# Optimization experiments

Measured on AMD Instinct MI355X. Metric: run time of the kernel, lower is better.

The kernel has to match this reference:

```python
import jax, jax.numpy as jnp
from jax import lax
import numpy as np


def _greedy_match(s):
    """Sequential greedy assignment on a single [N, N] score matrix.
    Mirrors Binary.forward for the n1=n2=None (square) case:
    repeat N times: pick global argmax, zero its row and column in the
    working copy, set perm[row, col] = 1.
    """
    N = s.shape[0]

    def step(carry, _):
        s_tmp, perm = carry
        idx = jnp.argmax(s_tmp)          # flat argmax over N*N
        r = idx // N
        c = idx % N
        s_tmp = s_tmp.at[r, :].set(0.0).at[:, c].set(0.0)
        perm = perm.at[r, c].set(1.0)
        return (s_tmp, perm), None

    (_, perm), _ = lax.scan(step, (s, jnp.zeros_like(s)), None, length=N)
    return perm


def setup_inputs() -> dict:
    key = jax.random.key(0)
    B, N = 256, 512
    s = jax.random.uniform(key, (B, N, N), dtype=jnp.float32)
    return {"s": s}


def reference(s):
    # vmap over batch; each batch element runs an independent sequential
    # greedy matching (the data-dependent part is the length-N scan).
    return jax.vmap(_greedy_match)(s)
```

## Files before the change

### kernel.cpp

```cpp
#include <hip/hip_runtime.h>

#define NN 512
#define BATCH 256
#define T 8
#define ATH 40

typedef unsigned long long u64;
typedef unsigned u32;
typedef unsigned char u8;
typedef unsigned short u16;

#define DEADK 512ull
#define LIVEMIN (1ull << 32)
#define UNKNOWN 0xFFFFu

__device__ __forceinline__ u64 fm(u64 a, u64 b) {
    return (u64)__double_as_longlong(fmax(__longlong_as_double((long long)a),
                                          __longlong_as_double((long long)b)));
}
__device__ __forceinline__ u64 fmn(u64 a, u64 b) {
    return (u64)__double_as_longlong(fmin(__longlong_as_double((long long)a),
                                          __longlong_as_double((long long)b)));
}

#define DPP_FMAX64(k, ctrl) do {                                              \
    int _lo = (int)(u32)(k); int _hi = (int)((k) >> 32);                      \
    int _olo = __builtin_amdgcn_update_dpp(_lo, _lo, ctrl, 0xf, 0xf, false);  \
    int _ohi = __builtin_amdgcn_update_dpp(_hi, _hi, ctrl, 0xf, 0xf, false);  \
    u64 _o = ((u64)(u32)_ohi << 32) | (u32)_olo;                              \
    (k) = fm((k), _o);                                                        \
} while (0)

#define WAVE_FMAX64(k) do {                                                   \
    DPP_FMAX64(k, 0x111); DPP_FMAX64(k, 0x112); DPP_FMAX64(k, 0x114);         \
    DPP_FMAX64(k, 0x118); DPP_FMAX64(k, 0x142); DPP_FMAX64(k, 0x143);         \
} while (0)

__device__ __forceinline__ u64 readlane64(u64 k, int l) {
    u32 lo = (u32)__builtin_amdgcn_readlane((int)(u32)k, l);
    u32 hi = (u32)__builtin_amdgcn_readlane((int)(k >> 32), l);
    return ((u64)hi << 32) | lo;
}

__device__ __forceinline__ u64 amsel(int w, u64 a0, u64 a1, u64 a2, u64 a3,
                                     u64 a4, u64 a5, u64 a6, u64 a7) {
    u64 x01 = (w & 1) ? a1 : a0;
    u64 x23 = (w & 1) ? a3 : a2;
    u64 x45 = (w & 1) ? a5 : a4;
    u64 x67 = (w & 1) ? a7 : a6;
    u64 y0 = (w & 2) ? x23 : x01;
    u64 y1 = (w & 2) ? x67 : x45;
    return (w & 4) ? y1 : y0;
}

#define INS8(X, A0, A1, A2, A3, A4, A5, A6, A7) do {                          \
    u64 _x = (X), _n;                                                         \
    _n = fm(A0, _x); _x = fmn(A0, _x); A0 = _n;                               \
    _n = fm(A1, _x); _x = fmn(A1, _x); A1 = _n;                               \
    _n = fm(A2, _x); _x = fmn(A2, _x); A2 = _n;                               \
    _n = fm(A3, _x); _x = fmn(A3, _x); A3 = _n;                               \
    _n = fm(A4, _x); _x = fmn(A4, _x); A4 = _n;                               \
    _n = fm(A5, _x); _x = fmn(A5, _x); A5 = _n;                               \
    _n = fm(A6, _x); _x = fmn(A6, _x); A6 = _n;                               \
    A7 = fm(A7, _x);                                                          \
} while (0)

#define ALIVE_C(cc) ((amsel((int)(cc) >> 6, am0,am1,am2,am3,am4,am5,am6,am7)  \
                      >> ((cc) & 63)) & 1ull)
#define ALIVE_R(rr) ((amsel((int)(rr) >> 6, ar0,ar1,ar2,ar3,ar4,ar5,ar6,ar7)  \
                      >> ((rr) & 63)) & 1ull)
#define SETK(RS, VAL) do {                                                    \
        const int rsl_ = (RS) & 63, rsj_ = (RS) >> 6;                         \
        const bool mn_ = (lane == rsl_);                                      \
        k0 = (mn_ && rsj_ == 0) ? (VAL) : k0;                                 \
        k1 = (mn_ && rsj_ == 1) ? (VAL) : k1;                                 \
        k2 = (mn_ && rsj_ == 2) ? (VAL) : k2;                                 \
        k3 = (mn_ && rsj_ == 3) ? (VAL) : k3;                                 \
        k4 = (mn_ && rsj_ == 4) ? (VAL) : k4;                                 \
        k5 = (mn_ && rsj_ == 5) ? (VAL) : k5;                                 \
        k6 = (mn_ && rsj_ == 6) ? (VAL) : k6;                                 \
        k7 = (mn_ && rsj_ == 7) ? (VAL) : k7;                                 \
    } while (0)

#define COLDROW(RR, NKVAR) do {                                               \
        const float* rp_ = sb + (size_t)(RR) * NN;                            \
        const float4 fa_ = *(const float4*)(rp_ + 4 * lane);                  \
        const float4 fv_ = *(const float4*)(rp_ + 256 + 4 * lane);            \
        const int sh_ = (4 * lane) & 63; const int wq_ = lane >> 4;           \
        u64 xlo_ = (wq_ == 0) ? am0 : (wq_ == 1) ? am1 : (wq_ == 2) ? am2 : am3; \
        u64 xhi_ = (wq_ == 0) ? am4 : (wq_ == 1) ? am5 : (wq_ == 2) ? am6 : am7; \
        const u32 al8_ = ((u32)(xlo_ >> sh_) & 0xFu)                          \
                       | (((u32)(xhi_ >> sh_) & 0xFu) << 4);                  \
        u64 e0_ = (al8_ & 1u)   ? ((((u64)__float_as_uint(fa_.x) + 1) << 9) | (u32)(511 - (4*lane+0))) : 0; \
        u64 e1_ = (al8_ & 2u)   ? ((((u64)__float_as_uint(fa_.y) + 1) << 9) | (u32)(511 - (4*lane+1))) : 0; \
        u64 e2_ = (al8_ & 4u)   ? ((((u64)__float_as_uint(fa_.z) + 1) << 9) | (u32)(511 - (4*lane+2))) : 0; \
        u64 e3_ = (al8_ & 8u)   ? ((((u64)__float_as_uint(fa_.w) + 1) << 9) | (u32)(511 - (4*lane+3))) : 0; \
        u64 e4_ = (al8_ & 16u)  ? ((((u64)__float_as_uint(fv_.x) + 1) << 9) | (u32)(511 - (256+4*lane+0))) : 0; \
        u64 e5_ = (al8_ & 32u)  ? ((((u64)__float_as_uint(fv_.y) + 1) << 9) | (u32)(511 - (256+4*lane+1))) : 0; \
        u64 e6_ = (al8_ & 64u)  ? ((((u64)__float_as_uint(fv_.z) + 1) << 9) | (u32)(511 - (256+4*lane+2))) : 0; \
        u64 e7_ = (al8_ & 128u) ? ((((u64)__float_as_uint(fv_.w) + 1) << 9) | (u32)(511 - (256+4*lane+3))) : 0; \
        u64 n0_ = fm(e0_, e1_), n1_ = fm(e2_, e3_);                           \
        u64 n2_ = fm(e4_, e5_), n3_ = fm(e6_, e7_);                           \
        n0_ = fm(n0_, n1_); n2_ = fm(n2_, n3_);                               \
        u64 bw_ = fm(n0_, n2_);                                               \
        WAVE_FMAX64(bw_);                                                     \
        bw_ = readlane64(bw_, 63);                                            \
        const int wc_ = 511 - (int)(bw_ & 511);                               \
        NKVAR = ((bw_ >> 9) << 32)                                            \
              | ((u64)(u32)(512 - (RR)) << 16) | (u32)wc_;                    \
        if (lane == 0)                                                        \
            rl[RR][7] = (((bw_ >> 9) - 1ull) << 32) | (u32)wc_;               \
    } while (0)

__global__ __launch_bounds__(256) void build_row(const float* __restrict__ s,
                                                 float* __restrict__ out) {
    const int b = blockIdx.x >> 3;
    const int rbase = (blockIdx.x & 7) * 64;
    const int t = threadIdx.x;
    const int ct = t & 63, q = t >> 6;

    __shared__ float tile[64][65];
    __shared__ u64 mrg[64][4][8];

    const float* sb = s + (size_t)b * NN * NN;

    u64 t0 = 0, t1 = 0, t2 = 0, t3 = 0, t4 = 0, t5 = 0, t6 = 0, t7 = 0;

    for (int ch = 0; ch < 8; ++ch) {
        const int cbase = ch * 64;
        #pragma unroll
        for (int i = 0; i < 16; ++i) {
            const int rr = q + 4 * i;
            tile[rr][ct] = sb[(size_t)(rbase + rr) * NN + cbase + ct];
        }
        __syncthreads();
        #pragma unroll
        for (int i = 0; i < 16; ++i) {
            const int cc = cbase + 16 * q + i;
            const float v = tile[ct][16 * q + i];
            const u64 x = (((u64)__float_as_uint(v) + 1) << 9) | (u32)(511 - cc);
            INS8(x, t0, t1, t2, t3, t4, t5, t6, t7);
        }
        __syncthreads();
    }

    mrg[ct][q][0] = t0;  mrg[ct][q][1] = t1;  mrg[ct][q][2] = t2;
    mrg[ct][q][3] = t3;  mrg[ct][q][4] = t4;  mrg[ct][q][5] = t5;
    mrg[ct][q][6] = t6;  mrg[ct][q][7] = t7;
    __syncthreads();

    if (t < 64) {
        u64 m0 = 0, m1 = 0, m2 = 0, m3 = 0, m4 = 0, m5 = 0, m6 = 0, m7 = 0;
        #pragma unroll
        for (int qq = 0; qq < 4; ++qq)
            #pragma unroll
            for (int ii = 0; ii < 8; ++ii) {
                const u64 x = mrg[t][qq][ii];
                INS8(x, m0, m1, m2, m3, m4, m5, m6, m7);
            }
        u64* dst = (u64*)(out + (size_t)b * NN * NN) + (size_t)(rbase + t) * T;
        dst[0] = (((m0 >> 9) - 1ull) << 32) | (u32)(511 - (int)(m0 & 511));
        dst[1] = (((m1 >> 9) - 1ull) << 32) | (u32)(511 - (int)(m1 & 511));
        dst[2] = (((m2 >> 9) - 1ull) << 32) | (u32)(511 - (int)(m2 & 511));
        dst[3] = (((m3 >> 9) - 1ull) << 32) | (u32)(511 - (int)(m3 & 511));
        dst[4] = (((m4 >> 9) - 1ull) << 32) | (u32)(511 - (int)(m4 & 511));
        dst[5] = (((m5 >> 9) - 1ull) << 32) | (u32)(511 - (int)(m5 & 511));
        dst[6] = (((m6 >> 9) - 1ull) << 32) | (u32)(511 - (int)(m6 & 511));
        dst[7] = (((m7 >> 9) - 1ull) << 32) | (u32)(511 - (int)(m7 & 511));
    }
}

__global__ __launch_bounds__(256) void build_col(const float* __restrict__ s,
                                                 float* __restrict__ out) {
    const int b = blockIdx.x >> 3;
    const int cbase = (blockIdx.x & 7) * 64;
    const int t = threadIdx.x;
    const int ct = t & 63, q = t >> 6;

    __shared__ float tile[64][65];
    __shared__ u64 mrg[64][4][8];

    const float* sb = s + (size_t)b * NN * NN;

    u64 t0 = 0, t1 = 0, t2 = 0, t3 = 0, t4 = 0, t5 = 0, t6 = 0, t7 = 0;

    for (int ch = 0; ch < 8; ++ch) {
        const int rbase = ch * 64;
        #pragma unroll
        for (int i = 0; i < 16; ++i) {
            const int rr = q + 4 * i;
            tile[rr][ct] = sb[(size_t)(rbase + rr) * NN + cbase + ct];
        }
        __syncthreads();
        #pragma unroll
        for (int i = 0; i < 16; ++i) {
            const int rr = rbase + q * 16 + i;
            const float v = tile[q * 16 + i][ct];
            const u64 x = (((u64)__float_as_uint(v) + 1) << 9) | (u32)(511 - rr);
            INS8(x, t0, t1, t2, t3, t4, t5, t6, t7);
        }
        __syncthreads();
    }

    mrg[ct][q][0] = t0;  mrg[ct][q][1] = t1;  mrg[ct][q][2] = t2;
    mrg[ct][q][3] = t3;  mrg[ct][q][4] = t4;  mrg[ct][q][5] = t5;
    mrg[ct][q][6] = t6;  mrg[ct][q][7] = t7;
    __syncthreads();

    if (t < 64) {
        u64 m0 = 0, m1 = 0, m2 = 0, m3 = 0, m4 = 0, m5 = 0, m6 = 0, m7 = 0;
        #pragma unroll
        for (int qq = 0; qq < 4; ++qq)
            #pragma unroll
            for (int ii = 0; ii < 8; ++ii) {
                const u64 x = mrg[t][qq][ii];
                INS8(x, m0, m1, m2, m3, m4, m5, m6, m7);
            }
        u64* dst = (u64*)(out + (size_t)b * NN * NN) + (size_t)NN * T
                 + (size_t)(cbase + t) * T;
        dst[0] = m0; dst[1] = m1; dst[2] = m2; dst[3] = m3;
        dst[4] = m4; dst[5] = m5; dst[6] = m6; dst[7] = m7;
    }
}

__global__ __launch_bounds__(256) void greedy_A(const float* __restrict__ s,
                                                float* __restrict__ out,
                                                u32* __restrict__ ws_mat) {
    __shared__ __align__(16) u64 rl[NN][9];
    __shared__ __align__(16) u64 cl[NN][9];
    __shared__ __align__(16) u64 keysL[NN];
    __shared__ u32 colh[NN];
    __shared__ u8 aliveR[NN];
    __shared__ u8 aliveC[NN];
    __shared__ u16 match16[NN];
    __shared__ int cntW[4];

    const int tid = threadIdx.x;
    const int w = tid >> 6, lane = tid & 63;
    const int b = blockIdx.x;
    const float* sb = s + (size_t)b * NN * NN;
    float* ob = out + (size_t)b * NN * NN;
    u64* st = (u64*)ob + 8192;

    {
        const ulonglong2* src = (const ulonglong2*)ob;
        #pragma unroll
        for (int i = 0; i < 8; ++i) {
            const int i2 = tid + 256 * i;
            const ulonglong2 vR = src[i2];
            const ulonglong2 vC = src[2048 + i2];
            const int idx = i2 * 2;
            rl[idx >> 3][idx & 7] = vR.x;  rl[idx >> 3][(idx & 7) + 1] = vR.y;
            cl[idx >> 3][idx & 7] = vC.x;  cl[idx >> 3][(idx & 7) + 1] = vC.y;
        }
    }
    if (tid < 128) {
        ((u32*)aliveR)[tid] = 0x01010101u;
        ((u32*)aliveC)[tid] = 0x01010101u;
    }
    match16[tid] = 0; match16[tid + 256] = 0;
    __syncthreads();
    #pragma unroll
    for (int i = 0; i < 2; ++i) {
        const int r = tid + 256 * i;
        const u64 e = rl[r][0];
        keysL[r] = (((e >> 32) + 1ull) << 32)
                 | ((u64)(u32)(512 - r) << 16) | (e & 511ull);
        colh[r] = 511u - ((u32)cl[r][0] & 511u);
    }
    __syncthreads();

    u64 am0 = ~0ull, am1 = ~0ull, am2 = ~0ull, am3 = ~0ull,
        am4 = ~0ull, am5 = ~0ull, am6 = ~0ull, am7 = ~0ull;
    u64 ar0 = ~0ull, ar1 = ~0ull, ar2 = ~0ull, ar3 = ~0ull,
        ar4 = ~0ull, ar5 = ~0ull, ar6 = ~0ull, ar7 = ~0ull;

    int alive = NN;

    #pragma unroll 1
    for (int round = 0; round < 64; ++round) {
        int part = 0;
        #pragma unroll
        for (int j = 0; j < 2; ++j) {
            const int row = 128 * w + 64 * j + lane;
            const u64 kj = keysL[row];
            const u32 cc = (u32)kj & 511u;
            const bool hit = (kj >= LIVEMIN) && (colh[cc] == (u32)row);
            part += (int)__builtin_popcountll(__ballot(hit));
            if (hit) {
                match16[row] = (u16)cc;
                aliveC[cc] = 0;
                aliveR[row] = 0;
                keysL[row] = DEADK;
            }
        }
        if (lane == 0) cntW[w] = part;
        __syncthreads();
        const int cnt = cntW[0] + cntW[1] + cntW[2] + cntW[3];
        if (cnt == 0) break;
        alive -= cnt;

        am0 = __ballot(aliveC[lane] != 0);        am1 = __ballot(aliveC[64 + lane] != 0);
        am2 = __ballot(aliveC[128 + lane] != 0);  am3 = __ballot(aliveC[192 + lane] != 0);
        am4 = __ballot(aliveC[256 + lane] != 0);  am5 = __ballot(aliveC[320 + lane] != 0);
        am6 = __ballot(aliveC[384 + lane] != 0);  am7 = __ballot(aliveC[448 + lane] != 0);
        ar0 = __ballot(aliveR[lane] != 0);        ar1 = __ballot(aliveR[64 + lane] != 0);
        ar2 = __ballot(aliveR[128 + lane] != 0);  ar3 = __ballot(aliveR[192 + lane] != 0);
        ar4 = __ballot(aliveR[256 + lane] != 0);  ar5 = __ballot(aliveR[320 + lane] != 0);
        ar6 = __ballot(aliveR[384 + lane] != 0);  ar7 = __ballot(aliveR[448 + lane] != 0);

        if (alive <= ATH) break;

        u32 coldR = 0;
        #pragma unroll
        for (int j = 0; j < 2; ++j) {
            const int row = 128 * w + 64 * j + lane;
            const u64 kj = keysL[row];
            if (kj >= LIVEMIN && !ALIVE_C((u32)kj & 511u)) {
                const u64 f0 = rl[row][0], f1 = rl[row][1], f2 = rl[row][2];
                const u64 f3 = rl[row][3], f4 = rl[row][4], f5 = rl[row][5];
                const u64 f6 = rl[row][6], f7 = rl[row][7];
                const u64 a0 = ALIVE_C((u32)f0 & 511u);
                const u64 a1 = ALIVE_C((u32)f1 & 511u);
                const u64 a2 = ALIVE_C((u32)f2 & 511u);
                const u64 a3 = ALIVE_C((u32)f3 & 511u);
                const u64 a4 = ALIVE_C((u32)f4 & 511u);
                const u64 a5 = ALIVE_C((u32)f5 & 511u);
                const u64 a6 = ALIVE_C((u32)f6 & 511u);
                const u64 a7 = ALIVE_C((u32)f7 & 511u);
                u64 sel = 0;
                sel = a7 ? f7 : sel; sel = a6 ? f6 : sel;
                sel = a5 ? f5 : sel; sel = a4 ? f4 : sel;
                sel = a3 ? f3 : sel; sel = a2 ? f2 : sel;
                sel = a1 ? f1 : sel; sel = a0 ? f0 : sel;
                if (a0 | a1 | a2 | a3 | a4 | a5 | a6 | a7) {
                    keysL[row] = ((sel >> 32) + 1ull) << 32
                               | ((u64)(u32)(512 - row) << 16) | (sel & 511ull);
                } else coldR |= 1u << j;
            }
        }
        u64 mk = __ballot(coldR != 0u);
        while (mk) {
            const int l = (int)__builtin_ctzll(mk); mk &= mk - 1;
            u32 lm = (u32)__builtin_amdgcn_readlane((int)coldR, l);
            while (lm) {
                const int jj = (int)__builtin_ctz(lm); lm &= lm - 1;
                const int r = 128 * w + 64 * jj + l;
                u64 nkc;
                COLDROW(r, nkc);
                if (lane == 0) keysL[r] = nkc;
            }
        }

        #pragma unroll
        for (int j = 0; j < 2; ++j) {
            const int c = 128 * w + 64 * j + lane;
            const u32 chv = colh[c];
            if (aliveC[c] && chv != UNKNOWN && !ALIVE_R(chv)) {
                const u64 g0 = cl[c][0], g1 = cl[c][1], g2 = cl[c][2];
                const u64 g3 = cl[c][3], g4 = cl[c][4], g5 = cl[c][5];
                const u64 g6 = cl[c][6], g7 = cl[c][7];
                const u64 b0 = ALIVE_R(511u - ((u32)g0 & 511u));
                const u64 b1 = ALIVE_R(511u - ((u32)g1 & 511u));
                const u64 b2 = ALIVE_R(511u - ((u32)g2 & 511u));
                const u64 b3 = ALIVE_R(511u - ((u32)g3 & 511u));
                const u64 b4 = ALIVE_R(511u - ((u32)g4 & 511u));
                const u64 b5 = ALIVE_R(511u - ((u32)g5 & 511u));
                const u64 b6 = ALIVE_R(511u - ((u32)g6 & 511u));
                const u64 b7 = ALIVE_R(511u - ((u32)g7 & 511u));
                u64 sel = 0;
                sel = b7 ? g7 : sel; sel = b6 ? g6 : sel;
                sel = b5 ? g5 : sel; sel = b4 ? g4 : sel;
                sel = b3 ? g3 : sel; sel = b2 ? g2 : sel;
                sel = b1 ? g1 : sel; sel = b0 ? g0 : sel;
                colh[c] = (b0 | b1 | b2 | b3 | b4 | b5 | b6 | b7)
                        ? (511u - ((u32)sel & 511u)) : UNKNOWN;
            }
        }
        __syncthreads();
    }

    __syncthreads();
    st[tid] = keysL[tid];
    st[tid + 256] = keysL[tid + 256];
    if (tid < 8)
        st[512 + tid] = amsel(tid, am0, am1, am2, am3, am4, am5, am6, am7);
    ws_mat[b * 256 + tid] = ((const u32*)match16)[tid];
}

__global__ __launch_bounds__(64) void greedy_B(const float* __restrict__ s,
                                               const float* __restrict__ out,
                                               u32* __restrict__ ws_mat) {
    __shared__ __align__(16) u64 rl[NN][8];
    __shared__ u16 match16[NN];

    const int b = blockIdx.x;
    const int lane = threadIdx.x;
    const float* sb = s + (size_t)b * NN * NN;
    const float* ob = out + (size_t)b * NN * NN;
    const u64* st = (const u64*)ob + 8192;

    {
        const ulonglong2* src = (const ulonglong2*)ob;
        ulonglong2* dstl = (ulonglong2*)&rl[0][0];
        #pragma unroll
        for (int j = 0; j < 32; ++j)
            dstl[lane + 64 * j] = src[lane + 64 * j];
    }
    {
        u32* m32 = (u32*)match16;
        #pragma unroll
        for (int i = 0; i < 4; ++i)
            m32[lane + 64 * i] = ws_mat[b * 256 + lane + 64 * i];
    }

    u64 am0 = st[512], am1 = st[513], am2 = st[514], am3 = st[515];
    u64 am4 = st[516], am5 = st[517], am6 = st[518], am7 = st[519];

    u64 k0 = st[lane];        u64 k1 = st[lane + 64];
    u64 k2 = st[lane + 128];  u64 k3 = st[lane + 192];
    u64 k4 = st[lane + 256];  u64 k5 = st[lane + 320];
    u64 k6 = st[lane + 384];  u64 k7 = st[lane + 448];

    int done = NN;
    done -= (int)__builtin_popcountll(__ballot(k0 >= LIVEMIN));
    done -= (int)__builtin_popcountll(__ballot(k1 >= LIVEMIN));
    done -= (int)__builtin_popcountll(__ballot(k2 >= LIVEMIN));
    done -= (int)__builtin_popcountll(__ballot(k3 >= LIVEMIN));
    done -= (int)__builtin_popcountll(__ballot(k4 >= LIVEMIN));
    done -= (int)__builtin_popcountll(__ballot(k5 >= LIVEMIN));
    done -= (int)__builtin_popcountll(__ballot(k6 >= LIVEMIN));
    done -= (int)__builtin_popcountll(__ballot(k7 >= LIVEMIN));

    #pragma unroll 1
    while (done < NN) {
        u64 m0 = fm(k0, k1), m1 = fm(k2, k3), m2 = fm(k4, k5), m3 = fm(k6, k7);
        m0 = fm(m0, m1); m2 = fm(m2, m3);
        u64 bk = fm(m0, m2);
        WAVE_FMAX64(bk);
        const u32 lo = (u32)__builtin_amdgcn_readlane((int)(u32)bk, 63);
        const int cstar = (int)(lo & 511u);
        const int rstar = 512 - (int)((lo >> 16) & 1023u);

        const u64 e = rl[rstar][lane & 7];
        const int cw = cstar >> 6;
        const u64 aw = amsel(cw, am0, am1, am2, am3, am4, am5, am6, am7);
        const bool valid = ((aw >> (cstar & 63)) & 1ull) != 0ull;

        u64 nk;
        if (valid) {
            if (lane == 0) match16[rstar] = (u16)cstar;
            const u64 nb = ~(1ull << (cstar & 63));
            am0 = (cw == 0) ? (am0 & nb) : am0;  am1 = (cw == 1) ? (am1 & nb) : am1;
            am2 = (cw == 2) ? (am2 & nb) : am2;  am3 = (cw == 3) ? (am3 & nb) : am3;
            am4 = (cw == 4) ? (am4 & nb) : am4;  am5 = (cw == 5) ? (am5 & nb) : am5;
            am6 = (cw == 6) ? (am6 & nb) : am6;  am7 = (cw == 7) ? (am7 & nb) : am7;
            nk = DEADK;
            ++done;
        } else {
            const int c = (int)(e & 511u);
            const u64 w = amsel(c >> 6, am0, am1, am2, am3, am4, am5, am6, am7);
            const bool al = ((w >> (c & 63)) & 1ull) != 0ull;
            const u64 mask = __ballot(al) & 0xFFull;
            if (mask) {
                const u64 es = readlane64(e, (int)__builtin_ctzll(mask));
                nk = (((es >> 32) + 1ull) << 32)
                   | ((u64)(u32)(512 - rstar) << 16) | (es & 511ull);
            } else {
                COLDROW(rstar, nk);
            }
        }
        SETK(rstar, nk);
    }

    {
        const u32* m32 = (const u32*)match16;
        #pragma unroll
        for (int i = 0; i < 4; ++i)
            ws_mat[b * 256 + lane + 64 * i] = m32[lane + 64 * i];
    }
}

__global__ __launch_bounds__(256) void write_out(const u32* __restrict__ ws_mat,
                                                 float* __restrict__ out) {
    const int gid = blockIdx.x * 256 + threadIdx.x;
    const int b = gid >> 16;
    const int rem = gid & 65535;
    const int row = rem >> 7;
    const int quad = rem & 127;
    const u32 w = ws_mat[b * 256 + (row >> 1)];
    const int c = (int)((w >> (16 * (row & 1))) & 0xFFFFu);
    float4 f;
    f.x = (c == quad * 4 + 0) ? 1.0f : 0.0f;
    f.y = (c == quad * 4 + 1) ? 1.0f : 0.0f;
    f.z = (c == quad * 4 + 2) ? 1.0f : 0.0f;
    f.w = (c == quad * 4 + 3) ? 1.0f : 0.0f;
    ((float4*)out)[gid] = f;
}

extern "C" void kernel_launch(void* const* d_in, const int* in_sizes, int n_in,
                              void* d_out, int out_size, void* d_ws, size_t ws_size,
                              hipStream_t stream) {
    const float* s = (const float*)d_in[0];
    float* out = (float*)d_out;
    u32* ws_mat = (u32*)d_ws;

    build_row<<<dim3(BATCH * 8), dim3(256), 0, stream>>>(s, out);
    build_col<<<dim3(BATCH * 8), dim3(256), 0, stream>>>(s, out);
    greedy_A<<<dim3(BATCH), dim3(256), 0, stream>>>(s, out, ws_mat);
    greedy_B<<<dim3(BATCH), dim3(64), 0, stream>>>(s, out, ws_mat);
    write_out<<<dim3(BATCH * 256), dim3(256), 0, stream>>>(ws_mat, out);
}
```

Before: 295.1 us.

## Fuse row and column top-8 builds into one pass with partial column merge

The separate row and column top-8 candidate kernels each read the full 256MB score tensor. They are replaced by one kernel that loads each 64x64 tile once and computes both per-row and per-strip per-column top-8 lists. The per-strip column partials go to scratch space in the output buffer and are merged by a small new kernel. This halves global reads of the input, at the cost of extra per-chunk syncs, shared-memory merges and partial-list writes.

```diff
diff --git a/kernel.cpp b/kernel.cpp
--- a/kernel.cpp
+++ b/kernel.cpp
@@ -112,10 +112,11 @@
             rl[RR][7] = (((bw_ >> 9) - 1ull) << 32) | (u32)wc_;               \
     } while (0)
 
-__global__ __launch_bounds__(256) void build_row(const float* __restrict__ s,
-                                                 float* __restrict__ out) {
+__global__ __launch_bounds__(256) void build_fused(const float* __restrict__ s,
+                                                   float* __restrict__ out) {
     const int b = blockIdx.x >> 3;
-    const int rbase = (blockIdx.x & 7) * 64;
+    const int strip = blockIdx.x & 7;
+    const int rbase = strip * 64;
     const int t = threadIdx.x;
     const int ct = t & 63, q = t >> 6;
 
@@ -123,8 +124,10 @@
     __shared__ u64 mrg[64][4][8];
 
     const float* sb = s + (size_t)b * NN * NN;
-
-    u64 t0 = 0, t1 = 0, t2 = 0, t3 = 0, t4 = 0, t5 = 0, t6 = 0, t7 = 0;
+    u64* slab = (u64*)(out + (size_t)b * NN * NN);
+    u64* part = slab + 16384 + (size_t)strip * 4096;
+
+    u64 r0 = 0, r1 = 0, r2 = 0, r3 = 0, r4 = 0, r5 = 0, r6 = 0, r7 = 0;
 
     for (int ch = 0; ch < 8; ++ch) {
         const int cbase = ch * 64;
@@ -134,19 +137,47 @@
             tile[rr][ct] = sb[(size_t)(rbase + rr) * NN + cbase + ct];
         }
         __syncthreads();
+
         #pragma unroll
         for (int i = 0; i < 16; ++i) {
             const int cc = cbase + 16 * q + i;
             const float v = tile[ct][16 * q + i];
             const u64 x = (((u64)__float_as_uint(v) + 1) << 9) | (u32)(511 - cc);
-            INS8(x, t0, t1, t2, t3, t4, t5, t6, t7);
-        }
+            INS8(x, r0, r1, r2, r3, r4, r5, r6, r7);
+        }
+
+        u64 c0 = 0, c1 = 0, c2 = 0, c3 = 0, c4 = 0, c5 = 0, c6 = 0, c7 = 0;
+        #pragma unroll
+        for (int i = 0; i < 16; ++i) {
+            const int rr = rbase + 16 * q + i;
+            const float v = tile[16 * q + i][ct];
+            const u64 x = (((u64)__float_as_uint(v) + 1) << 9) | (u32)(511 - rr);
+            INS8(x, c0, c1, c2, c3, c4, c5, c6, c7);
+        }
+        mrg[ct][q][0] = c0;  mrg[ct][q][1] = c1;  mrg[ct][q][2] = c2;
+        mrg[ct][q][3] = c3;  mrg[ct][q][4] = c4;  mrg[ct][q][5] = c5;
+        mrg[ct][q][6] = c6;  mrg[ct][q][7] = c7;
         __syncthreads();
-    }
-
-    mrg[ct][q][0] = t0;  mrg[ct][q][1] = t1;  mrg[ct][q][2] = t2;
-    mrg[ct][q][3] = t3;  mrg[ct][q][4] = t4;  mrg[ct][q][5] = t5;
-    mrg[ct][q][6] = t6;  mrg[ct][q][7] = t7;
+
+        if (t < 64) {
+            u64 m0 = 0, m1 = 0, m2 = 0, m3 = 0, m4 = 0, m5 = 0, m6 = 0, m7 = 0;
+            #pragma unroll
+            for (int qq = 0; qq < 4; ++qq)
+                #pragma unroll
+                for (int ii = 0; ii < 8; ++ii) {
+                    const u64 x = mrg[t][qq][ii];
+                    INS8(x, m0, m1, m2, m3, m4, m5, m6, m7);
+                }
+            u64* dst = part + (size_t)(cbase + t) * 8;
+            dst[0] = m0; dst[1] = m1; dst[2] = m2; dst[3] = m3;
+            dst[4] = m4; dst[5] = m5; dst[6] = m6; dst[7] = m7;
+        }
+        __syncthreads();
+    }
+
+    mrg[ct][q][0] = r0;  mrg[ct][q][1] = r1;  mrg[ct][q][2] = r2;
+    mrg[ct][q][3] = r3;  mrg[ct][q][4] = r4;  mrg[ct][q][5] = r5;
+    mrg[ct][q][6] = r6;  mrg[ct][q][7] = r7;
     __syncthreads();
 
     if (t < 64) {
@@ -158,7 +189,7 @@
                 const u64 x = mrg[t][qq][ii];
                 INS8(x, m0, m1, m2, m3, m4, m5, m6, m7);
             }
-        u64* dst = (u64*)(out + (size_t)b * NN * NN) + (size_t)(rbase + t) * T;
+        u64* dst = slab + (size_t)(rbase + t) * T;
         dst[0] = (((m0 >> 9) - 1ull) << 32) | (u32)(511 - (int)(m0 & 511));
         dst[1] = (((m1 >> 9) - 1ull) << 32) | (u32)(511 - (int)(m1 & 511));
         dst[2] = (((m2 >> 9) - 1ull) << 32) | (u32)(511 - (int)(m2 & 511));
@@ -170,57 +201,25 @@
     }
 }
 
-__global__ __launch_bounds__(256) void build_col(const float* __restrict__ s,
-                                                 float* __restrict__ out) {
-    const int b = blockIdx.x >> 3;
-    const int cbase = (blockIdx.x & 7) * 64;
-    const int t = threadIdx.x;
-    const int ct = t & 63, q = t >> 6;
-
-    __shared__ float tile[64][65];
-    __shared__ u64 mrg[64][4][8];
-
-    const float* sb = s + (size_t)b * NN * NN;
-
-    u64 t0 = 0, t1 = 0, t2 = 0, t3 = 0, t4 = 0, t5 = 0, t6 = 0, t7 = 0;
-
-    for (int ch = 0; ch < 8; ++ch) {
-        const int rbase = ch * 64;
-        #pragma unroll
-        for (int i = 0; i < 16; ++i) {
-            const int rr = q + 4 * i;
-            tile[rr][ct] = sb[(size_t)(rbase + rr) * NN + cbase + ct];
-        }
-        __syncthreads();
-        #pragma unroll
-        for (int i = 0; i < 16; ++i) {
-            const int rr = rbase + q * 16 + i;
-            const float v = tile[q * 16 + i][ct];
-            const u64 x = (((u64)__float_as_uint(v) + 1) << 9) | (u32)(511 - rr);
-            INS8(x, t0, t1, t2, t3, t4, t5, t6, t7);
-        }
-        __syncthreads();
-    }
-
-    mrg[ct][q][0] = t0;  mrg[ct][q][1] = t1;  mrg[ct][q][2] = t2;
-    mrg[ct][q][3] = t3;  mrg[ct][q][4] = t4;  mrg[ct][q][5] = t5;
-    mrg[ct][q][6] = t6;  mrg[ct][q][7] = t7;
-    __syncthreads();
-
-    if (t < 64) {
-        u64 m0 = 0, m1 = 0, m2 = 0, m3 = 0, m4 = 0, m5 = 0, m6 = 0, m7 = 0;
-        #pragma unroll
-        for (int qq = 0; qq < 4; ++qq)
-            #pragma unroll
-            for (int ii = 0; ii < 8; ++ii) {
-                const u64 x = mrg[t][qq][ii];
-                INS8(x, m0, m1, m2, m3, m4, m5, m6, m7);
-            }
-        u64* dst = (u64*)(out + (size_t)b * NN * NN) + (size_t)NN * T
-                 + (size_t)(cbase + t) * T;
-        dst[0] = m0; dst[1] = m1; dst[2] = m2; dst[3] = m3;
-        dst[4] = m4; dst[5] = m5; dst[6] = m6; dst[7] = m7;
-    }
+__global__ __launch_bounds__(256) void merge_col(float* __restrict__ out) {
+    const int b = blockIdx.x >> 1;
+    const int c = ((blockIdx.x & 1) << 8) + threadIdx.x;
+    u64* slab = (u64*)(out + (size_t)b * NN * NN);
+    const u64* part = slab + 16384;
+
+    u64 m0 = 0, m1 = 0, m2 = 0, m3 = 0, m4 = 0, m5 = 0, m6 = 0, m7 = 0;
+    #pragma unroll
+    for (int st = 0; st < 8; ++st) {
+        const u64* p = part + (size_t)st * 4096 + (size_t)c * 8;
+        #pragma unroll
+        for (int i = 0; i < 8; ++i) {
+            const u64 x = p[i];
+            INS8(x, m0, m1, m2, m3, m4, m5, m6, m7);
+        }
+    }
+    u64* dst = slab + (size_t)NN * T + (size_t)c * T;
+    dst[0] = m0; dst[1] = m1; dst[2] = m2; dst[3] = m3;
+    dst[4] = m4; dst[5] = m5; dst[6] = m6; dst[7] = m7;
 }
 
 __global__ __launch_bounds__(256) void greedy_A(const float* __restrict__ s,
@@ -505,8 +504,8 @@
     float* out = (float*)d_out;
     u32* ws_mat = (u32*)d_ws;
 
-    build_row<<<dim3(BATCH * 8), dim3(256), 0, stream>>>(s, out);
-    build_col<<<dim3(BATCH * 8), dim3(256), 0, stream>>>(s, out);
+    build_fused<<<dim3(BATCH * 8), dim3(256), 0, stream>>>(s, out);
+    merge_col<<<dim3(BATCH * 2), dim3(256), 0, stream>>>(out);
     greedy_A<<<dim3(BATCH), dim3(256), 0, stream>>>(s, out, ws_mat);
     greedy_B<<<dim3(BATCH), dim3(64), 0, stream>>>(s, out, ws_mat);
     write_out<<<dim3(BATCH * 256), dim3(256), 0, stream>>>(ws_mat, out);
```

Result: slower. 317.1 us (+7.4%).
